# Kernel optimization log

Hardware: AMD Instinct MI355X
Metric: run time of the kernel (lower is better)

## Reference

```python
import jax, jax.numpy as jnp
import numpy as np

N_HEADS, D_MODEL, D_HEAD = 16, 1024, 64
BATCH, SEQ = 2, 2048
INIT_RANGE = 0.02


def setup_inputs() -> dict:
    key = jax.random.key(0)
    ks = jax.random.split(key, 5)
    x = jax.random.normal(ks[0], (BATCH, SEQ, D_MODEL), dtype=jnp.float32)
    W_Q = jax.random.normal(ks[1], (N_HEADS, D_MODEL, D_HEAD), dtype=jnp.float32) * INIT_RANGE
    W_K = jax.random.normal(ks[2], (N_HEADS, D_MODEL, D_HEAD), dtype=jnp.float32) * INIT_RANGE
    W_V = jax.random.normal(ks[3], (N_HEADS, D_MODEL, D_HEAD), dtype=jnp.float32) * INIT_RANGE
    W_O = jax.random.normal(ks[4], (N_HEADS, D_HEAD, D_MODEL), dtype=jnp.float32) * INIT_RANGE
    b_Q = jnp.zeros((N_HEADS, D_HEAD), dtype=jnp.float32)
    b_K = jnp.zeros((N_HEADS, D_HEAD), dtype=jnp.float32)
    b_V = jnp.zeros((N_HEADS, D_HEAD), dtype=jnp.float32)
    b_O = jnp.zeros((D_MODEL,), dtype=jnp.float32)
    return {"normalized_resid_pre": x, "W_Q": W_Q, "W_K": W_K, "W_V": W_V,
            "W_O": W_O, "b_Q": b_Q, "b_K": b_K, "b_V": b_V, "b_O": b_O}


def reference(normalized_resid_pre, W_Q, W_K, W_V, W_O, b_Q, b_K, b_V, b_O):
    x = normalized_resid_pre  # [b, s, d_model]
    q = jnp.einsum('bsm,hmd->bshd', x, W_Q) + b_Q  # [b, s, h, d_head]
    k = jnp.einsum('bsm,hmd->bshd', x, W_K) + b_K
    v = jnp.einsum('bsm,hmd->bshd', x, W_V) + b_V
    scores = jnp.einsum('bqhd,bkhd->bhqk', q, k) / jnp.sqrt(jnp.float32(D_HEAD))
    seq = x.shape[1]
    causal = jnp.tril(jnp.ones((seq, seq), dtype=bool))  # True where allowed
    scores = jnp.where(causal, scores, jnp.float32(-jnp.inf))
    pattern = jax.nn.softmax(scores, axis=-1)  # [b, h, q, k]
    z = jnp.einsum('bhqk,bkhd->bqhd', pattern, v)
    attn_out = jnp.einsum('bqhd,hdm->bqm', z, W_O) + b_O
    return attn_out
```

## Files before the change

### kernel.cpp

```cpp
#include <hip/hip_runtime.h>
#include <hip/hip_bf16.h>

#define BATCH 2
#define SEQL 2048
#define NH 16
#define DH 64
#define DM 1024
#define LDK 72
#define QSCALE 0.1803368801111244f

typedef __hip_bfloat16 bf16;
typedef __attribute__((ext_vector_type(8)))  short bf16x8;
typedef __attribute__((ext_vector_type(4)))  float f32x4;

__device__ __forceinline__ void gl_lds16(const void* g, void* l) {
    __builtin_amdgcn_global_load_lds(
        (const __attribute__((address_space(1))) unsigned int*)g,
        (__attribute__((address_space(3))) unsigned int*)l, 16, 0, 0);
}

__global__ __launch_bounds__(256) void prep_kernel(
    const float* __restrict__ x,
    const float* __restrict__ Wq, const float* __restrict__ Wk,
    const float* __restrict__ Wv, const float* __restrict__ Wo,
    bf16* __restrict__ Wt, bf16* __restrict__ xb)
{
    const int zi = blockIdx.z;
    if (zi == 4) {
        const int bid = blockIdx.y * 16 + blockIdx.x;
        const size_t base = ((size_t)bid * 256 + threadIdx.x) * 4;
        #pragma unroll
        for (int it = 0; it < 16; ++it) {
            const size_t i = base + (size_t)it * 262144;
            const float4 v = *(const float4*)(x + i);
            bf16 o[4];
            o[0] = __float2bfloat16(v.x); o[1] = __float2bfloat16(v.y);
            o[2] = __float2bfloat16(v.z); o[3] = __float2bfloat16(v.w);
            *(uint2*)(xb + i) = *(const uint2*)o;
        }
        return;
    }

    __shared__ float ts[64][65];
    const float* src = (zi == 0) ? Wq : (zi == 1) ? Wk : (zi == 2) ? Wv : Wo;
    bf16* dst = Wt + (size_t)zi * DM * DM;
    const int row0 = blockIdx.y * 64;
    const int col0 = blockIdx.x * 64;
    const int tx = threadIdx.x & 63;
    const int ty = threadIdx.x >> 6;

    if (zi < 3) {
        const int h = col0 >> 6;
        #pragma unroll
        for (int i = 0; i < 16; ++i) {
            const int r = ty + 4 * i;
            ts[r][tx] = src[h * (DM * DH) + (row0 + r) * DH + tx];
        }
    } else {
        #pragma unroll
        for (int i = 0; i < 16; ++i) {
            const int r = ty + 4 * i;
            ts[r][tx] = src[(size_t)(row0 + r) * DM + col0 + tx];
        }
    }
    __syncthreads();
    #pragma unroll
    for (int i = 0; i < 16; ++i) {
        const int rr = ty + 4 * i;
        dst[(size_t)(col0 + rr) * DM + row0 + tx] = __float2bfloat16(ts[tx][rr]);
    }
}

__global__ __launch_bounds__(256) void qkv_gemm(
    const bf16* __restrict__ xb, const bf16* __restrict__ Wt,
    const float* __restrict__ bq, const float* __restrict__ bk, const float* __restrict__ bv,
    bf16* __restrict__ qkv)
{
    __shared__ __align__(16) bf16 As[2][128 * 32];
    __shared__ __align__(16) bf16 Bs[2][128 * 32];

    const int t = threadIdx.x;
    const int lane = t & 63, w = t >> 6;
    const int ml = lane & 15, quad = lane >> 4;
    const int wr = w >> 1, wc = w & 1;
    const int bid0 = blockIdx.y * 8 + blockIdx.x;
    const int L = (bid0 & 7) * 32 + (bid0 >> 3);
    const int bn = L & 7, bm = L >> 3;
    const int which = blockIdx.z;

    const bf16* A0 = xb + (size_t)(bm * 128) * DM;
    const bf16* B0 = Wt + (size_t)which * DM * DM + (size_t)(bn * 128) * DM;
    const float* bias = (which == 0) ? bq : (which == 1) ? bk : bv;
    bf16* outb = qkv + (size_t)which * (BATCH * SEQL * NH * DH);
    const float oscale = (which == 0) ? QSCALE : 1.0f;

    f32x4 acc[4][4];
    #pragma unroll
    for (int i = 0; i < 4; ++i)
        #pragma unroll
        for (int j = 0; j < 4; ++j) acc[i][j] = (f32x4){0.f, 0.f, 0.f, 0.f};

    const int r0 = t >> 2, c0 = (t & 3) * 8;
    const int f1 = t + 256;
    const int r1 = f1 >> 2, c1 = (f1 & 3) * 8;

    for (int kt = 0; kt < DM / 64; ++kt) {
        const int k0 = kt * 64;
        __syncthreads();
        #pragma unroll
        for (int half = 0; half < 2; ++half) {
            const int kh = k0 + half * 32;
            gl_lds16(A0 + (size_t)r0 * DM + kh + c0, &As[half][t * 8]);
            gl_lds16(A0 + (size_t)r1 * DM + kh + c1, &As[half][f1 * 8]);
            gl_lds16(B0 + (size_t)r0 * DM + kh + c0, &Bs[half][t * 8]);
            gl_lds16(B0 + (size_t)r1 * DM + kh + c1, &Bs[half][f1 * 8]);
        }
        __syncthreads();
        #pragma unroll
        for (int half = 0; half < 2; ++half) {
            bf16x8 af[4], bfr[4];
            #pragma unroll
            for (int i = 0; i < 4; ++i)
                af[i] = *(const bf16x8*)&As[half][(wr * 64 + i * 16 + ml) * 32 + quad * 8];
            #pragma unroll
            for (int j = 0; j < 4; ++j)
                bfr[j] = *(const bf16x8*)&Bs[half][(wc * 64 + j * 16 + ml) * 32 + quad * 8];
            #pragma unroll
            for (int i = 0; i < 4; ++i)
                #pragma unroll
                for (int j = 0; j < 4; ++j)
                    acc[i][j] = __builtin_amdgcn_mfma_f32_16x16x32_bf16(af[i], bfr[j], acc[i][j], 0, 0, 0);
        }
    }

    float bb[4];
    #pragma unroll
    for (int j = 0; j < 4; ++j) bb[j] = bias[bn * 128 + wc * 64 + j * 16 + ml];

    if (which == 2) {
        #pragma unroll
        for (int i = 0; i < 4; ++i) {
            const int row0v = bm * 128 + wr * 64 + i * 16 + quad * 4;
            const int b = row0v >> 11;
            const int s0 = row0v & (SEQL - 1);
            #pragma unroll
            for (int j = 0; j < 4; ++j) {
                const int col = bn * 128 + wc * 64 + j * 16 + ml;
                const int h = col >> 6, d = col & 63;
                bf16 tmp[4];
                #pragma unroll
                for (int rg = 0; rg < 4; ++rg)
                    tmp[rg] = __float2bfloat16(acc[i][j][rg] + bb[j]);
                *(uint2*)&outb[(((size_t)(b * NH + h)) * DH + d) * SEQL + s0] =
                    *(const uint2*)tmp;
            }
        }
    } else {
        #pragma unroll
        for (int i = 0; i < 4; ++i) {
            #pragma unroll
            for (int rg = 0; rg < 4; ++rg) {
                const int row = bm * 128 + wr * 64 + i * 16 + quad * 4 + rg;
                const int b = row >> 11;
                const int s = row & (SEQL - 1);
                #pragma unroll
                for (int j = 0; j < 4; ++j) {
                    const int col = bn * 128 + wc * 64 + j * 16 + ml;
                    const int h = col >> 6, d = col & 63;
                    outb[(((size_t)(b * NH + h)) * SEQL + s) * DH + d] =
                        __float2bfloat16((acc[i][j][rg] + bb[j]) * oscale);
                }
            }
        }
    }
}

__global__ __launch_bounds__(256) void oproj_gemm(
    const bf16* __restrict__ zb, const bf16* __restrict__ Bt,
    const float* __restrict__ bo, float* __restrict__ out)
{
    __shared__ __align__(16) bf16 As[2][128 * 32];
    __shared__ __align__(16) bf16 Bs[2][64 * 32];

    const int t = threadIdx.x;
    const int lane = t & 63, w = t >> 6;
    const int ml = lane & 15, quad = lane >> 4;
    const int wr = w >> 1, wc = w & 1;
    const int bid0 = blockIdx.y * 16 + blockIdx.x;
    const int L = (bid0 & 7) * 64 + (bid0 >> 3);
    const int bn = L & 15, bm = L >> 4;

    const bf16* A0 = zb + (size_t)(bm * 128) * DM;
    const bf16* B0 = Bt + (size_t)(bn * 64) * DM;

    f32x4 acc[4][2];
    #pragma unroll
    for (int i = 0; i < 4; ++i)
        #pragma unroll
        for (int j = 0; j < 2; ++j) acc[i][j] = (f32x4){0.f, 0.f, 0.f, 0.f};

    const int r0 = t >> 2, c0 = (t & 3) * 8;
    const int f1 = t + 256;
    const int r1 = f1 >> 2, c1 = (f1 & 3) * 8;

    for (int kt = 0; kt < DM / 64; ++kt) {
        const int k0 = kt * 64;
        __syncthreads();
        #pragma unroll
        for (int half = 0; half < 2; ++half) {
            const int kh = k0 + half * 32;
            gl_lds16(A0 + (size_t)r0 * DM + kh + c0, &As[half][t * 8]);
            gl_lds16(A0 + (size_t)r1 * DM + kh + c1, &As[half][f1 * 8]);
            gl_lds16(B0 + (size_t)r0 * DM + kh + c0, &Bs[half][t * 8]);
        }
        __syncthreads();
        #pragma unroll
        for (int half = 0; half < 2; ++half) {
            bf16x8 af[4], bfr[2];
            #pragma unroll
            for (int i = 0; i < 4; ++i)
                af[i] = *(const bf16x8*)&As[half][(wr * 64 + i * 16 + ml) * 32 + quad * 8];
            #pragma unroll
            for (int j = 0; j < 2; ++j)
                bfr[j] = *(const bf16x8*)&Bs[half][(wc * 32 + j * 16 + ml) * 32 + quad * 8];
            #pragma unroll
            for (int i = 0; i < 4; ++i)
                #pragma unroll
                for (int j = 0; j < 2; ++j)
                    acc[i][j] = __builtin_amdgcn_mfma_f32_16x16x32_bf16(af[i], bfr[j], acc[i][j], 0, 0, 0);
        }
    }

    float bb[2];
    #pragma unroll
    for (int j = 0; j < 2; ++j) bb[j] = bo[bn * 64 + wc * 32 + j * 16 + ml];

    #pragma unroll
    for (int i = 0; i < 4; ++i) {
        #pragma unroll
        for (int rg = 0; rg < 4; ++rg) {
            const int row = bm * 128 + wr * 64 + i * 16 + quad * 4 + rg;
            #pragma unroll
            for (int j = 0; j < 2; ++j) {
                const int col = bn * 64 + wc * 32 + j * 16 + ml;
                out[(size_t)row * DM + col] = acc[i][j][rg] + bb[j];
            }
        }
    }
}

__global__ __launch_bounds__(512) void attn_kernel(
    const bf16* __restrict__ qg, const bf16* __restrict__ kg, const bf16* __restrict__ vtg,
    bf16* __restrict__ z)
{
    __shared__ __align__(16) bf16 KsS[128 * 64];
    __shared__ __align__(16) bf16 VtS[64 * 128];
    __shared__ __align__(16) bf16 PsS[8][16 * LDK];

    const int t    = threadIdx.x;
    const int lane = t & 63;
    const int w    = t >> 6;
    const int m    = lane & 15;
    const int quad = lane >> 4;
    const int wg   = w & 3;
    const int half = w >> 2;

    const int bid0 = blockIdx.y * 32 + blockIdx.x;
    const int L = (bid0 & 7) * 64 + (bid0 >> 3);
    const int bh = L >> 4;
    const int qa = L & 15;
    const int b  = bh >> 4;
    const int h  = bh & 15;
    const int qb = 31 - qa;
    const int q0a = qa * 64;
    const int q0b = qb * 64;

    const size_t base   = (size_t)bh * SEQL * DH;
    const size_t vtbase = (size_t)bh * DH * SEQL;

    const int s0 = t, s1 = t + 512;
    const int kr0 = s0 >> 3, kc0 = (s0 & 7) ^ (kr0 & 7);
    const int kr1 = s1 >> 3, kc1 = (s1 & 7) ^ (kr1 & 7);
    const int vr0 = s0 >> 4, vc0 = (s0 & 15) ^ (vr0 & 15);
    const int vr1 = s1 >> 4, vc1 = (s1 & 15) ^ (vr1 & 15);

    bf16x8 aq[2], aqB[2];
    {
        const int myq = (w < 4) ? (q0a + w * 16) : (q0b + wg * 16);
        const bf16* qp = qg + base + (size_t)(myq + m) * DH + quad * 8;
        aq[0] = *(const bf16x8*)(qp);
        aq[1] = *(const bf16x8*)(qp + 32);
        const bf16* qpb = qg + base + (size_t)(q0b + wg * 16 + m) * DH + quad * 8;
        aqB[0] = *(const bf16x8*)(qpb);
        aqB[1] = *(const bf16x8*)(qpb + 32);
    }

    const short ob = (m == 0) ? (short)0x3F80 : (short)0;
    const bf16x8 bones = {ob, ob, ob, ob, ob, ob, ob, ob};

    f32x4 zacc[4];
    #pragma unroll
    for (int nt = 0; nt < 4; ++nt) zacc[nt] = (f32x4){0.f, 0.f, 0.f, 0.f};
    f32x4 lacc = (f32x4){0.f, 0.f, 0.f, 0.f};

    bf16* Psw = PsS[w];

    const int CB = (qb >> 1) + 1;
    for (int c = 0; c < CB; ++c) {
        __syncthreads();
        {
            const int kc = c * 128;
            gl_lds16(kg + base + (size_t)(kc + kr0) * DH + kc0 * 8, &KsS[s0 * 8]);
            gl_lds16(kg + base + (size_t)(kc + kr1) * DH + kc1 * 8, &KsS[s1 * 8]);
            gl_lds16(vtg + vtbase + (size_t)vr0 * SEQL + kc + vc0 * 8, &VtS[s0 * 8]);
            gl_lds16(vtg + vtbase + (size_t)vr1 * SEQL + kc + vc1 * 8, &VtS[s1 * 8]);
        }
        __syncthreads();

        #pragma unroll
        for (int c2 = 0; c2 < 2; ++c2) {
            const int kt = 2 * c + c2;
            if (kt > qb) break;
            const int co = c2 * 64;

            if (kt <= qa) {
                f32x4 sc[4];
                #pragma unroll
                for (int nt = 0; nt < 4; ++nt) sc[nt] = (f32x4){0.f, 0.f, 0.f, 0.f};
                __builtin_amdgcn_s_setprio(1);
                #pragma unroll
                for (int ks = 0; ks < 2; ++ks) {
                    #pragma unroll
                    for (int nt = 0; nt < 4; ++nt) {
                        const int rw = co + nt * 16 + m;
                        const int pc = ((ks << 2) + quad) ^ (m & 7);
                        const bf16x8 bk = *(const bf16x8*)(&KsS[rw * 64 + pc * 8]);
                        sc[nt] = __builtin_amdgcn_mfma_f32_16x16x32_bf16(aq[ks], bk, sc[nt], 0, 0, 0);
                    }
                }
                __builtin_amdgcn_s_setprio(0);
                if (kt == qa && w < 4) {
                    #pragma unroll
                    for (int nt = 0; nt < 4; ++nt) {
                        const int col = nt * 16 + m;
                        #pragma unroll
                        for (int rg = 0; rg < 4; ++rg) {
                            const int row = wg * 16 + quad * 4 + rg;
                            if (col > row) sc[nt][rg] = -1e30f;
                        }
                    }
                }

                #pragma unroll
                for (int nt = 0; nt < 4; ++nt)
                    #pragma unroll
                    for (int rg = 0; rg < 4; ++rg)
                        Psw[(quad * 4 + rg) * LDK + nt * 16 + m] =
                            __float2bfloat16(__builtin_exp2f(sc[nt][rg]));

                __builtin_amdgcn_s_setprio(1);
                #pragma unroll
                for (int ks = 0; ks < 2; ++ks) {
                    const bf16x8 ap = *(const bf16x8*)(&Psw[m * LDK + ks * 32 + quad * 8]);
                    lacc = __builtin_amdgcn_mfma_f32_16x16x32_bf16(ap, bones, lacc, 0, 0, 0);
                    #pragma unroll
                    for (int nt = 0; nt < 4; ++nt) {
                        const int dr = nt * 16 + m;
                        const int vc = (c2 * 8 + (ks << 2) + quad) ^ m;
                        const bf16x8 bv = *(const bf16x8*)(&VtS[dr * 128 + vc * 8]);
                        zacc[nt] = __builtin_amdgcn_mfma_f32_16x16x32_bf16(ap, bv, zacc[nt], 0, 0, 0);
                    }
                }
                __builtin_amdgcn_s_setprio(0);

                if (kt == qa && w < 4) {
                    float invl[4];
                    #pragma unroll
                    for (int rg = 0; rg < 4; ++rg)
                        invl[rg] = 1.f / __shfl(lacc[rg], quad * 16);
                    #pragma unroll
                    for (int nt = 0; nt < 4; ++nt) {
                        const int d = nt * 16 + m;
                        #pragma unroll
                        for (int rg = 0; rg < 4; ++rg) {
                            const int qrow = q0a + wg * 16 + quad * 4 + rg;
                            z[(((size_t)b * SEQL + qrow) * NH + h) * DH + d] =
                                __float2bfloat16(zacc[nt][rg] * invl[rg]);
                        }
                    }
                    #pragma unroll
                    for (int nt = 0; nt < 4; ++nt) zacc[nt] = (f32x4){0.f, 0.f, 0.f, 0.f};
                    lacc = (f32x4){0.f, 0.f, 0.f, 0.f};
                    aq[0] = aqB[0]; aq[1] = aqB[1];
                }
            } else {
                f32x4 sc[2];
                sc[0] = (f32x4){0.f, 0.f, 0.f, 0.f};
                sc[1] = (f32x4){0.f, 0.f, 0.f, 0.f};
                __builtin_amdgcn_s_setprio(1);
                #pragma unroll
                for (int ks = 0; ks < 2; ++ks) {
                    #pragma unroll
                    for (int nt = 0; nt < 2; ++nt) {
                        const int rw = co + half * 32 + nt * 16 + m;
                        const int pc = ((ks << 2) + quad) ^ (m & 7);
                        const bf16x8 bk = *(const bf16x8*)(&KsS[rw * 64 + pc * 8]);
                        sc[nt] = __builtin_amdgcn_mfma_f32_16x16x32_bf16(aq[ks], bk, sc[nt], 0, 0, 0);
                    }
                }
                __builtin_amdgcn_s_setprio(0);
                if (kt == qb) {
                    #pragma unroll
                    for (int nt = 0; nt < 2; ++nt) {
                        const int col = half * 32 + nt * 16 + m;
                        #pragma unroll
                        for (int rg = 0; rg < 4; ++rg) {
                            const int row = wg * 16 + quad * 4 + rg;
                            if (col > row) sc[nt][rg] = -1e30f;
                        }
                    }
                }

                #pragma unroll
                for (int nt = 0; nt < 2; ++nt)
                    #pragma unroll
                    for (int rg = 0; rg < 4; ++rg)
                        Psw[(quad * 4 + rg) * LDK + nt * 16 + m] =
                            __float2bfloat16(__builtin_exp2f(sc[nt][rg]));

                __builtin_amdgcn_s_setprio(1);
                {
                    const bf16x8 ap = *(const bf16x8*)(&Psw[m * LDK + quad * 8]);
                    lacc = __builtin_amdgcn_mfma_f32_16x16x32_bf16(ap, bones, lacc, 0, 0, 0);
                    #pragma unroll
                    for (int nt = 0; nt < 4; ++nt) {
                        const int dr = nt * 16 + m;
                        const int vc = (c2 * 8 + (half << 2) + quad) ^ m;
                        const bf16x8 bv = *(const bf16x8*)(&VtS[dr * 128 + vc * 8]);
                        zacc[nt] = __builtin_amdgcn_mfma_f32_16x16x32_bf16(ap, bv, zacc[nt], 0, 0, 0);
                    }
                }
                __builtin_amdgcn_s_setprio(0);
            }
        }
    }

    __syncthreads();
    if (w < 4) {
        float* zs = (w < 2) ? ((float*)KsS) + (size_t)w * 1024
                            : ((float*)VtS) + (size_t)(w - 2) * 1024;
        #pragma unroll
        for (int nt = 0; nt < 4; ++nt)
            #pragma unroll
            for (int rg = 0; rg < 4; ++rg)
                zs[lane * 16 + nt * 4 + rg] = zacc[nt][rg];
        float* ls = ((float*)PsS) + w * 256;
        #pragma unroll
        for (int rg = 0; rg < 4; ++rg) ls[lane * 4 + rg] = lacc[rg];
    }
    __syncthreads();
    if (w >= 4) {
        const int ww = w - 4;
        const float* zs = (ww < 2) ? ((const float*)KsS) + (size_t)ww * 1024
                                   : ((const float*)VtS) + (size_t)(ww - 2) * 1024;
        const float* ls = ((const float*)PsS) + ww * 256;
        #pragma unroll
        for (int nt = 0; nt < 4; ++nt)
            #pragma unroll
            for (int rg = 0; rg < 4; ++rg)
                zacc[nt][rg] += zs[lane * 16 + nt * 4 + rg];
        #pragma unroll
        for (int rg = 0; rg < 4; ++rg) lacc[rg] += ls[lane * 4 + rg];

        float invl[4];
        #pragma unroll
        for (int rg = 0; rg < 4; ++rg)
            invl[rg] = 1.f / __shfl(lacc[rg], quad * 16);
        #pragma unroll
        for (int nt = 0; nt < 4; ++nt) {
            const int d = nt * 16 + m;
            #pragma unroll
            for (int rg = 0; rg < 4; ++rg) {
                const int qrow = q0b + wg * 16 + quad * 4 + rg;
                z[(((size_t)b * SEQL + qrow) * NH + h) * DH + d] =
                    __float2bfloat16(zacc[nt][rg] * invl[rg]);
            }
        }
    }
}

extern "C" void kernel_launch(void* const* d_in, const int* in_sizes, int n_in,
                              void* d_out, int out_size, void* d_ws, size_t ws_size,
                              hipStream_t stream)
{
    const float* x  = (const float*)d_in[0];
    const float* Wq = (const float*)d_in[1];
    const float* Wk = (const float*)d_in[2];
    const float* Wv = (const float*)d_in[3];
    const float* Wo = (const float*)d_in[4];
    const float* bq = (const float*)d_in[5];
    const float* bk = (const float*)d_in[6];
    const float* bv = (const float*)d_in[7];
    const float* bo = (const float*)d_in[8];
    float* out = (float*)d_out;

    const size_t TOK = (size_t)BATCH * SEQL;
    const size_t QKV = TOK * DM;
    bf16* xb  = (bf16*)d_ws;
    bf16* Wt  = xb + QKV;
    bf16* qkv = Wt + 4 * (size_t)DM * DM;
    bf16* zb  = qkv + 3 * QKV;

    prep_kernel<<<dim3(16, 16, 5), 256, 0, stream>>>(x, Wq, Wk, Wv, Wo, Wt, xb);
    qkv_gemm<<<dim3(8, 32, 3), 256, 0, stream>>>(xb, Wt, bq, bk, bv, qkv);
    attn_kernel<<<dim3(32, 16), 512, 0, stream>>>(
        qkv, qkv + QKV, qkv + 2 * QKV, zb);
    oproj_gemm<<<dim3(16, 32), 256, 0, stream>>>(zb, Wt + 3 * (size_t)DM * DM, bo, out);
}
```

Before: 183.9 us.

## Process 128-row query tiles per block with double-buffered K/V staging

The attention kernel now gives each wave two 64-row query groups, so every K/V fragment read from LDS feeds twice as many MFMAs. The grid is halved, with one block per (batch, head) and mirrored query-tile pair, and the block-index swizzle is dropped. K/V tiles are prefetched into a second LDS buffer while the current one is computed, which removes one barrier per iteration and overlaps global loads with compute. In exchange, register and LDS pressure roughly double, and the smaller grid gives less parallelism to hide latency and balance load across CUs.

```diff
diff --git a/kernel.cpp b/kernel.cpp
--- a/kernel.cpp
+++ b/kernel.cpp
@@ -249,13 +249,13 @@
     }
 }
 
-__global__ __launch_bounds__(512) void attn_kernel(
+__global__ __launch_bounds__(512, 2) void attn_kernel(
     const bf16* __restrict__ qg, const bf16* __restrict__ kg, const bf16* __restrict__ vtg,
     bf16* __restrict__ z)
 {
-    __shared__ __align__(16) bf16 KsS[128 * 64];
-    __shared__ __align__(16) bf16 VtS[64 * 128];
-    __shared__ __align__(16) bf16 PsS[8][16 * LDK];
+    __shared__ __align__(16) bf16 KsS[2][128 * 64];
+    __shared__ __align__(16) bf16 VtS[2][64 * 128];
+    __shared__ __align__(16) bf16 PsS[8][32 * LDK];
 
     const int t    = threadIdx.x;
     const int lane = t & 63;
@@ -265,15 +265,12 @@
     const int wg   = w & 3;
     const int half = w >> 2;
 
-    const int bid0 = blockIdx.y * 32 + blockIdx.x;
-    const int L = (bid0 & 7) * 64 + (bid0 >> 3);
-    const int bh = L >> 4;
-    const int qa = L & 15;
-    const int b  = bh >> 4;
+    const int bh = blockIdx.x;
+    const int b0 = bh >> 4;
     const int h  = bh & 15;
-    const int qb = 31 - qa;
-    const int q0a = qa * 64;
-    const int q0b = qb * 64;
+    const int pa = blockIdx.y;
+    const int pb = 15 - pa;
+    const int lastA = 2 * pa + 1;
 
     const size_t base   = (size_t)bh * SEQL * DH;
     const size_t vtbase = (size_t)bh * DH * SEQL;
@@ -284,49 +281,68 @@
     const int vr0 = s0 >> 4, vc0 = (s0 & 15) ^ (vr0 & 15);
     const int vr1 = s1 >> 4, vc1 = (s1 & 15) ^ (vr1 & 15);
 
-    bf16x8 aq[2], aqB[2];
-    {
-        const int myq = (w < 4) ? (q0a + w * 16) : (q0b + wg * 16);
-        const bf16* qp = qg + base + (size_t)(myq + m) * DH + quad * 8;
-        aq[0] = *(const bf16x8*)(qp);
-        aq[1] = *(const bf16x8*)(qp + 32);
-        const bf16* qpb = qg + base + (size_t)(q0b + wg * 16 + m) * DH + quad * 8;
-        aqB[0] = *(const bf16x8*)(qpb);
-        aqB[1] = *(const bf16x8*)(qpb + 32);
+    const int myTile0 = (w < 4) ? pa : pb;
+    int tile = myTile0;
+
+    bf16x8 aq[2][2], aqB[2][2];
+    #pragma unroll
+    for (int g = 0; g < 2; ++g) {
+        const bf16* qp = qg + base +
+            (size_t)(myTile0 * 128 + g * 64 + wg * 16 + m) * DH + quad * 8;
+        aq[g][0] = *(const bf16x8*)(qp);
+        aq[g][1] = *(const bf16x8*)(qp + 32);
+        const bf16* qpb = qg + base +
+            (size_t)(pb * 128 + g * 64 + wg * 16 + m) * DH + quad * 8;
+        aqB[g][0] = *(const bf16x8*)(qpb);
+        aqB[g][1] = *(const bf16x8*)(qpb + 32);
     }
 
     const short ob = (m == 0) ? (short)0x3F80 : (short)0;
     const bf16x8 bones = {ob, ob, ob, ob, ob, ob, ob, ob};
 
-    f32x4 zacc[4];
-    #pragma unroll
-    for (int nt = 0; nt < 4; ++nt) zacc[nt] = (f32x4){0.f, 0.f, 0.f, 0.f};
-    f32x4 lacc = (f32x4){0.f, 0.f, 0.f, 0.f};
+    f32x4 zacc[2][4];
+    f32x4 lacc[2];
+    #pragma unroll
+    for (int g = 0; g < 2; ++g) {
+        #pragma unroll
+        for (int nt = 0; nt < 4; ++nt) zacc[g][nt] = (f32x4){0.f, 0.f, 0.f, 0.f};
+        lacc[g] = (f32x4){0.f, 0.f, 0.f, 0.f};
+    }
 
     bf16* Psw = PsS[w];
 
-    const int CB = (qb >> 1) + 1;
+    const int CB = 16 - pa;
+
+    gl_lds16(kg + base + (size_t)kr0 * DH + kc0 * 8, &KsS[0][s0 * 8]);
+    gl_lds16(kg + base + (size_t)kr1 * DH + kc1 * 8, &KsS[0][s1 * 8]);
+    gl_lds16(vtg + vtbase + (size_t)vr0 * SEQL + vc0 * 8, &VtS[0][s0 * 8]);
+    gl_lds16(vtg + vtbase + (size_t)vr1 * SEQL + vc1 * 8, &VtS[0][s1 * 8]);
+
     for (int c = 0; c < CB; ++c) {
         __syncthreads();
-        {
-            const int kc = c * 128;
-            gl_lds16(kg + base + (size_t)(kc + kr0) * DH + kc0 * 8, &KsS[s0 * 8]);
-            gl_lds16(kg + base + (size_t)(kc + kr1) * DH + kc1 * 8, &KsS[s1 * 8]);
-            gl_lds16(vtg + vtbase + (size_t)vr0 * SEQL + kc + vc0 * 8, &VtS[s0 * 8]);
-            gl_lds16(vtg + vtbase + (size_t)vr1 * SEQL + kc + vc1 * 8, &VtS[s1 * 8]);
-        }
-        __syncthreads();
+        if (c + 1 < CB) {
+            const int kc = (c + 1) * 128;
+            bf16* Kd = &KsS[(c + 1) & 1][0];
+            bf16* Vd = &VtS[(c + 1) & 1][0];
+            gl_lds16(kg + base + (size_t)(kc + kr0) * DH + kc0 * 8, Kd + s0 * 8);
+            gl_lds16(kg + base + (size_t)(kc + kr1) * DH + kc1 * 8, Kd + s1 * 8);
+            gl_lds16(vtg + vtbase + (size_t)vr0 * SEQL + kc + vc0 * 8, Vd + s0 * 8);
+            gl_lds16(vtg + vtbase + (size_t)vr1 * SEQL + kc + vc1 * 8, Vd + s1 * 8);
+        }
+        const bf16* Ks = &KsS[c & 1][0];
+        const bf16* Vt = &VtS[c & 1][0];
 
         #pragma unroll
         for (int c2 = 0; c2 < 2; ++c2) {
             const int kt = 2 * c + c2;
-            if (kt > qb) break;
             const int co = c2 * 64;
 
-            if (kt <= qa) {
-                f32x4 sc[4];
-                #pragma unroll
-                for (int nt = 0; nt < 4; ++nt) sc[nt] = (f32x4){0.f, 0.f, 0.f, 0.f};
+            if (kt <= lastA) {
+                f32x4 sc[2][4];
+                #pragma unroll
+                for (int g = 0; g < 2; ++g)
+                    #pragma unroll
+                    for (int nt = 0; nt < 4; ++nt) sc[g][nt] = (f32x4){0.f, 0.f, 0.f, 0.f};
                 __builtin_amdgcn_s_setprio(1);
                 #pragma unroll
                 for (int ks = 0; ks < 2; ++ks) {
@@ -334,69 +350,85 @@
                     for (int nt = 0; nt < 4; ++nt) {
                         const int rw = co + nt * 16 + m;
                         const int pc = ((ks << 2) + quad) ^ (m & 7);
-                        const bf16x8 bk = *(const bf16x8*)(&KsS[rw * 64 + pc * 8]);
-                        sc[nt] = __builtin_amdgcn_mfma_f32_16x16x32_bf16(aq[ks], bk, sc[nt], 0, 0, 0);
+                        const bf16x8 bk = *(const bf16x8*)(&Ks[rw * 64 + pc * 8]);
+                        sc[0][nt] = __builtin_amdgcn_mfma_f32_16x16x32_bf16(aq[0][ks], bk, sc[0][nt], 0, 0, 0);
+                        sc[1][nt] = __builtin_amdgcn_mfma_f32_16x16x32_bf16(aq[1][ks], bk, sc[1][nt], 0, 0, 0);
                     }
                 }
                 __builtin_amdgcn_s_setprio(0);
-                if (kt == qa && w < 4) {
-                    #pragma unroll
-                    for (int nt = 0; nt < 4; ++nt) {
-                        const int col = nt * 16 + m;
-                        #pragma unroll
-                        for (int rg = 0; rg < 4; ++rg) {
-                            const int row = wg * 16 + quad * 4 + rg;
-                            if (col > row) sc[nt][rg] = -1e30f;
+
+                #pragma unroll
+                for (int g = 0; g < 2; ++g) {
+                    if (kt >= 2 * tile + g) {
+                        #pragma unroll
+                        for (int nt = 0; nt < 4; ++nt) {
+                            const int kv = kt * 64 + nt * 16 + m;
+                            #pragma unroll
+                            for (int rg = 0; rg < 4; ++rg) {
+                                const int qr = tile * 128 + g * 64 + wg * 16 + quad * 4 + rg;
+                                if (kv > qr) sc[g][nt][rg] = -1e30f;
+                            }
                         }
                     }
                 }
 
                 #pragma unroll
-                for (int nt = 0; nt < 4; ++nt)
-                    #pragma unroll
-                    for (int rg = 0; rg < 4; ++rg)
-                        Psw[(quad * 4 + rg) * LDK + nt * 16 + m] =
-                            __float2bfloat16(__builtin_exp2f(sc[nt][rg]));
+                for (int g = 0; g < 2; ++g)
+                    #pragma unroll
+                    for (int nt = 0; nt < 4; ++nt)
+                        #pragma unroll
+                        for (int rg = 0; rg < 4; ++rg)
+                            Psw[(g * 16 + quad * 4 + rg) * LDK + nt * 16 + m] =
+                                __float2bfloat16(__builtin_exp2f(sc[g][nt][rg]));
 
                 __builtin_amdgcn_s_setprio(1);
                 #pragma unroll
                 for (int ks = 0; ks < 2; ++ks) {
-                    const bf16x8 ap = *(const bf16x8*)(&Psw[m * LDK + ks * 32 + quad * 8]);
-                    lacc = __builtin_amdgcn_mfma_f32_16x16x32_bf16(ap, bones, lacc, 0, 0, 0);
+                    const bf16x8 ap0 = *(const bf16x8*)(&Psw[(m) * LDK + ks * 32 + quad * 8]);
+                    const bf16x8 ap1 = *(const bf16x8*)(&Psw[(16 + m) * LDK + ks * 32 + quad * 8]);
+                    lacc[0] = __builtin_amdgcn_mfma_f32_16x16x32_bf16(ap0, bones, lacc[0], 0, 0, 0);
+                    lacc[1] = __builtin_amdgcn_mfma_f32_16x16x32_bf16(ap1, bones, lacc[1], 0, 0, 0);
                     #pragma unroll
                     for (int nt = 0; nt < 4; ++nt) {
                         const int dr = nt * 16 + m;
                         const int vc = (c2 * 8 + (ks << 2) + quad) ^ m;
-                        const bf16x8 bv = *(const bf16x8*)(&VtS[dr * 128 + vc * 8]);
-                        zacc[nt] = __builtin_amdgcn_mfma_f32_16x16x32_bf16(ap, bv, zacc[nt], 0, 0, 0);
+                        const bf16x8 bv = *(const bf16x8*)(&Vt[dr * 128 + vc * 8]);
+                        zacc[0][nt] = __builtin_amdgcn_mfma_f32_16x16x32_bf16(ap0, bv, zacc[0][nt], 0, 0, 0);
+                        zacc[1][nt] = __builtin_amdgcn_mfma_f32_16x16x32_bf16(ap1, bv, zacc[1][nt], 0, 0, 0);
                     }
                 }
                 __builtin_amdgcn_s_setprio(0);
 
-                if (kt == qa && w < 4) {
-                    float invl[4];
-                    #pragma unroll
-                    for (int rg = 0; rg < 4; ++rg)
-                        invl[rg] = 1.f / __shfl(lacc[rg], quad * 16);
-                    #pragma unroll
-                    for (int nt = 0; nt < 4; ++nt) {
-                        const int d = nt * 16 + m;
-                        #pragma unroll
-                        for (int rg = 0; rg < 4; ++rg) {
-                            const int qrow = q0a + wg * 16 + quad * 4 + rg;
-                            z[(((size_t)b * SEQL + qrow) * NH + h) * DH + d] =
-                                __float2bfloat16(zacc[nt][rg] * invl[rg]);
+                if (kt == lastA && w < 4) {
+                    #pragma unroll
+                    for (int g = 0; g < 2; ++g) {
+                        float invl[4];
+                        #pragma unroll
+                        for (int rg = 0; rg < 4; ++rg)
+                            invl[rg] = 1.f / __shfl(lacc[g][rg], quad * 16);
+                        #pragma unroll
+                        for (int nt = 0; nt < 4; ++nt) {
+                            const int d = nt * 16 + m;
+                            #pragma unroll
+                            for (int rg = 0; rg < 4; ++rg) {
+                                const int qrow = pa * 128 + g * 64 + wg * 16 + quad * 4 + rg;
+                                z[(((size_t)b0 * SEQL + qrow) * NH + h) * DH + d] =
+                                    __float2bfloat16(zacc[g][nt][rg] * invl[rg]);
+                            }
                         }
-                    }
-                    #pragma unroll
-                    for (int nt = 0; nt < 4; ++nt) zacc[nt] = (f32x4){0.f, 0.f, 0.f, 0.f};
-                    lacc = (f32x4){0.f, 0.f, 0.f, 0.f};
-                    aq[0] = aqB[0]; aq[1] = aqB[1];
+                        #pragma unroll
+                        for (int nt = 0; nt < 4; ++nt) zacc[g][nt] = (f32x4){0.f, 0.f, 0.f, 0.f};
+                        lacc[g] = (f32x4){0.f, 0.f, 0.f, 0.f};
+                        aq[g][0] = aqB[g][0]; aq[g][1] = aqB[g][1];
+                    }
+                    tile = pb;
                 }
             } else {
-                f32x4 sc[2];
-                sc[0] = (f32x4){0.f, 0.f, 0.f, 0.f};
-                sc[1] = (f32x4){0.f, 0.f, 0.f, 0.f};
+                f32x4 sc[2][2];
+                #pragma unroll
+                for (int g = 0; g < 2; ++g)
+                    #pragma unroll
+                    for (int nt = 0; nt < 2; ++nt) sc[g][nt] = (f32x4){0.f, 0.f, 0.f, 0.f};
                 __builtin_amdgcn_s_setprio(1);
                 #pragma unroll
                 for (int ks = 0; ks < 2; ++ks) {
@@ -404,40 +436,50 @@
                     for (int nt = 0; nt < 2; ++nt) {
                         const int rw = co + half * 32 + nt * 16 + m;
                         const int pc = ((ks << 2) + quad) ^ (m & 7);
-                        const bf16x8 bk = *(const bf16x8*)(&KsS[rw * 64 + pc * 8]);
-                        sc[nt] = __builtin_amdgcn_mfma_f32_16x16x32_bf16(aq[ks], bk, sc[nt], 0, 0, 0);
+                        const bf16x8 bk = *(const bf16x8*)(&Ks[rw * 64 + pc * 8]);
+                        sc[0][nt] = __builtin_amdgcn_mfma_f32_16x16x32_bf16(aq[0][ks], bk, sc[0][nt], 0, 0, 0);
+                        sc[1][nt] = __builtin_amdgcn_mfma_f32_16x16x32_bf16(aq[1][ks], bk, sc[1][nt], 0, 0, 0);
                     }
                 }
                 __builtin_amdgcn_s_setprio(0);
-                if (kt == qb) {
-                    #pragma unroll
-                    for (int nt = 0; nt < 2; ++nt) {
-                        const int col = half * 32 + nt * 16 + m;
-                        #pragma unroll
-                        for (int rg = 0; rg < 4; ++rg) {
-                            const int row = wg * 16 + quad * 4 + rg;
-                            if (col > row) sc[nt][rg] = -1e30f;
+
+                #pragma unroll
+                for (int g = 0; g < 2; ++g) {
+                    if (kt >= 2 * pb + g) {
+                        #pragma unroll
+                        for (int nt = 0; nt < 2; ++nt) {
+                            const int kv = kt * 64 + half * 32 + nt * 16 + m;
+                            #pragma unroll
+                            for (int rg = 0; rg < 4; ++rg) {
+                                const int qr = pb * 128 + g * 64 + wg * 16 + quad * 4 + rg;
+                                if (kv > qr) sc[g][nt][rg] = -1e30f;
+                            }
                         }
                     }
                 }
 
                 #pragma unroll
-                for (int nt = 0; nt < 2; ++nt)
-                    #pragma unroll
-                    for (int rg = 0; rg < 4; ++rg)
-                        Psw[(quad * 4 + rg) * LDK + nt * 16 + m] =
-                            __float2bfloat16(__builtin_exp2f(sc[nt][rg]));
+                for (int g = 0; g < 2; ++g)
+                    #pragma unroll
+                    for (int nt = 0; nt < 2; ++nt)
+                        #pragma unroll
+                        for (int rg = 0; rg < 4; ++rg)
+                            Psw[(g * 16 + quad * 4 + rg) * LDK + nt * 16 + m] =
+                                __float2bfloat16(__builtin_exp2f(sc[g][nt][rg]));
 
                 __builtin_amdgcn_s_setprio(1);
                 {
-                    const bf16x8 ap = *(const bf16x8*)(&Psw[m * LDK + quad * 8]);
-                    lacc = __builtin_amdgcn_mfma_f32_16x16x32_bf16(ap, bones, lacc, 0, 0, 0);
+                    const bf16x8 ap0 = *(const bf16x8*)(&Psw[(m) * LDK + quad * 8]);
+                    const bf16x8 ap1 = *(const bf16x8*)(&Psw[(16 + m) * LDK + quad * 8]);
+                    lacc[0] = __builtin_amdgcn_mfma_f32_16x16x32_bf16(ap0, bones, lacc[0], 0, 0, 0);
+                    lacc[1] = __builtin_amdgcn_mfma_f32_16x16x32_bf16(ap1, bones, lacc[1], 0, 0, 0);
                     #pragma unroll
                     for (int nt = 0; nt < 4; ++nt) {
                         const int dr = nt * 16 + m;
                         const int vc = (c2 * 8 + (half << 2) + quad) ^ m;
-                        const bf16x8 bv = *(const bf16x8*)(&VtS[dr * 128 + vc * 8]);
-                        zacc[nt] = __builtin_amdgcn_mfma_f32_16x16x32_bf16(ap, bv, zacc[nt], 0, 0, 0);
+                        const bf16x8 bv = *(const bf16x8*)(&Vt[dr * 128 + vc * 8]);
+                        zacc[0][nt] = __builtin_amdgcn_mfma_f32_16x16x32_bf16(ap0, bv, zacc[0][nt], 0, 0, 0);
+                        zacc[1][nt] = __builtin_amdgcn_mfma_f32_16x16x32_bf16(ap1, bv, zacc[1][nt], 0, 0, 0);
                     }
                 }
                 __builtin_amdgcn_s_setprio(0);
@@ -447,43 +489,49 @@
 
     __syncthreads();
     if (w < 4) {
-        float* zs = (w < 2) ? ((float*)KsS) + (size_t)w * 1024
-                            : ((float*)VtS) + (size_t)(w - 2) * 1024;
-        #pragma unroll
-        for (int nt = 0; nt < 4; ++nt)
+        float* zs = (float*)KsS + (size_t)w * 2048;
+        float* ls = (float*)VtS + (size_t)w * 512;
+        #pragma unroll
+        for (int g = 0; g < 2; ++g) {
+            #pragma unroll
+            for (int nt = 0; nt < 4; ++nt)
+                #pragma unroll
+                for (int rg = 0; rg < 4; ++rg)
+                    zs[((g * 4 + nt) * 4 + rg) * 64 + lane] = zacc[g][nt][rg];
             #pragma unroll
             for (int rg = 0; rg < 4; ++rg)
-                zs[lane * 16 + nt * 4 + rg] = zacc[nt][rg];
-        float* ls = ((float*)PsS) + w * 256;
-        #pragma unroll
-        for (int rg = 0; rg < 4; ++rg) ls[lane * 4 + rg] = lacc[rg];
+                ls[(g * 4 + rg) * 64 + lane] = lacc[g][rg];
+        }
     }
     __syncthreads();
     if (w >= 4) {
         const int ww = w - 4;
-        const float* zs = (ww < 2) ? ((const float*)KsS) + (size_t)ww * 1024
-                                   : ((const float*)VtS) + (size_t)(ww - 2) * 1024;
-        const float* ls = ((const float*)PsS) + ww * 256;
-        #pragma unroll
-        for (int nt = 0; nt < 4; ++nt)
+        const float* zs = (const float*)KsS + (size_t)ww * 2048;
+        const float* ls = (const float*)VtS + (size_t)ww * 512;
+        #pragma unroll
+        for (int g = 0; g < 2; ++g) {
+            #pragma unroll
+            for (int nt = 0; nt < 4; ++nt)
+                #pragma unroll
+                for (int rg = 0; rg < 4; ++rg)
+                    zacc[g][nt][rg] += zs[((g * 4 + nt) * 4 + rg) * 64 + lane];
             #pragma unroll
             for (int rg = 0; rg < 4; ++rg)
-                zacc[nt][rg] += zs[lane * 16 + nt * 4 + rg];
-        #pragma unroll
-        for (int rg = 0; rg < 4; ++rg) lacc[rg] += ls[lane * 4 + rg];
-
-        float invl[4];
-        #pragma unroll
-        for (int rg = 0; rg < 4; ++rg)
-            invl[rg] = 1.f / __shfl(lacc[rg], quad * 16);
-        #pragma unroll
-        for (int nt = 0; nt < 4; ++nt) {
-            const int d = nt * 16 + m;
-            #pragma unroll
-            for (int rg = 0; rg < 4; ++rg) {
-                const int qrow = q0b + wg * 16 + quad * 4 + rg;
-                z[(((size_t)b * SEQL + qrow) * NH + h) * DH + d] =
-                    __float2bfloat16(zacc[nt][rg] * invl[rg]);
+                lacc[g][rg] += ls[(g * 4 + rg) * 64 + lane];
+
+            float invl[4];
+            #pragma unroll
+            for (int rg = 0; rg < 4; ++rg)
+                invl[rg] = 1.f / __shfl(lacc[g][rg], quad * 16);
+            #pragma unroll
+            for (int nt = 0; nt < 4; ++nt) {
+                const int d = nt * 16 + m;
+                #pragma unroll
+                for (int rg = 0; rg < 4; ++rg) {
+                    const int qrow = pb * 128 + g * 64 + wg * 16 + quad * 4 + rg;
+                    z[(((size_t)b0 * SEQL + qrow) * NH + h) * DH + d] =
+                        __float2bfloat16(zacc[g][nt][rg] * invl[rg]);
+                }
             }
         }
     }
@@ -513,7 +561,7 @@
 
     prep_kernel<<<dim3(16, 16, 5), 256, 0, stream>>>(x, Wq, Wk, Wv, Wo, Wt, xb);
     qkv_gemm<<<dim3(8, 32, 3), 256, 0, stream>>>(xb, Wt, bq, bk, bv, qkv);
-    attn_kernel<<<dim3(32, 16), 512, 0, stream>>>(
+    attn_kernel<<<dim3(BATCH * NH, 8), 512, 0, stream>>>(
         qkv, qkv + QKV, qkv + 2 * QKV, zb);
     oproj_gemm<<<dim3(16, 32), 256, 0, stream>>>(zb, Wt + 3 * (size_t)DM * DM, bo, out);
 }
```

Result: no change. 181.8 us (-1.1%).
